# Kernel optimization log

Measured on AMD Instinct MI355X. Metric: run time of the kernel, lower is better.

The kernel has to match this reference:

```python
import jax, jax.numpy as jnp
import numpy as np
from jax import lax

SCORE_THRESHOLD = 0.5
IOU_THRESHOLD = 0.5
N_ANCHORS = 8400


def setup_inputs() -> dict:
    key = jax.random.key(0)
    yolo_raw_output = jax.random.uniform(key, (1, 5, N_ANCHORS), dtype=jnp.float32)
    return {"yolo_raw_output": yolo_raw_output}


def _pairwise_iou(boxes):
    # boxes: [N, 4] in xyxy
    x1, y1, x2, y2 = boxes[:, 0], boxes[:, 1], boxes[:, 2], boxes[:, 3]
    area = (x2 - x1) * (y2 - y1)                       # [N]
    lt_x = jnp.maximum(x1[:, None], x1[None, :])       # [N, N]
    lt_y = jnp.maximum(y1[:, None], y1[None, :])
    rb_x = jnp.minimum(x2[:, None], x2[None, :])
    rb_y = jnp.minimum(y2[:, None], y2[None, :])
    inter = jnp.clip(rb_x - lt_x, 0.0) * jnp.clip(rb_y - lt_y, 0.0)
    union = area[:, None] + area[None, :] - inter
    return inter / union


def reference(yolo_raw_output):
    # [1, 5, N] -> [N, 5]
    out = jnp.transpose(yolo_raw_output, (0, 2, 1))[0]
    scores = out[:, 4]
    valid = scores > SCORE_THRESHOLD            # score filter (mask, fixed shape)

    # cxcywh -> xyxy
    cx, cy, w, h = out[:, 0], out[:, 1], out[:, 2], out[:, 3]
    xyxy = jnp.stack([cx - w * 0.5, cy - h * 0.5, cx + w * 0.5, cy + h * 0.5], axis=1)

    # sort by score descending (invalid pushed to the end)
    masked_scores = jnp.where(valid, scores, -jnp.inf)
    order = jnp.argsort(-masked_scores)
    boxes_s = xyxy[order]                       # [N, 4]
    scores_s = jnp.where(valid, scores, 0.0)[order]
    valid_s = valid[order]

    # NMS: pairwise IoU + sequential suppression over sorted boxes
    iou = _pairwise_iou(lax.stop_gradient(boxes_s))
    suppress = iou > IOU_THRESHOLD              # [N, N] bool
    idx = jnp.arange(boxes_s.shape[0])

    def body(i, keep):
        # box i suppresses later boxes only if it itself is kept
        sup = suppress[i] & keep[i] & (idx > i)
        return keep & ~sup

    keep = lax.fori_loop(0, boxes_s.shape[0], body, valid_s)

    boxes_and_scores = jnp.concatenate([boxes_s, scores_s[:, None]], axis=1)  # [N, 5]
    # fixed-shape analogue of boxes_and_scores[selected_indices]:
    # suppressed / below-threshold rows are zeroed, kept rows are score-sorted.
    return jnp.where(keep[:, None], boxes_and_scores, 0.0)
```

## Files before the change

### kernel.cpp

```cpp
#include <hip/hip_runtime.h>
#include <cstdint>

#define N_ANCH 8400
#define WMAX   132
#define NB     (WMAX * 64)
#define NT     128

__device__ __forceinline__ uint64_t readlane64(uint64_t v, int lane) {
  unsigned lo = (unsigned)__builtin_amdgcn_readlane((int)(unsigned)(v & 0xffffffffull), lane);
  unsigned hi = (unsigned)__builtin_amdgcn_readlane((int)(unsigned)(v >> 32), lane);
  return ((uint64_t)hi << 32) | lo;
}

__global__ __launch_bounds__(256) void k_rank(const float* __restrict__ in,
                                              float* __restrict__ scores_s,
                                              float4* __restrict__ boxes_s,
                                              unsigned* __restrict__ nvp) {
  __shared__ alignas(16) float sc[N_ANCH];
  __shared__ int part[256];
  const int tid = threadIdx.x;
  const float* srow = in + 4 * N_ANCH;
  for (int j = tid; j < N_ANCH; j += 256) sc[j] = srow[j];
  __syncthreads();
  const int il = tid & 63, q = tid >> 6;
  const int i = blockIdx.x * 64 + il;
  const float si = (i < N_ANCH) ? sc[i] : 0.0f;
  const bool valid = si > 0.5f;
  const float key = valid ? si : -INFINITY;
  int cnt = 0;
  const float4* sc4 = (const float4*)sc;
  const int jb = q * (N_ANCH / 4);
  for (int jj = 0; jj < (N_ANCH / 16); ++jj) {
    float4 v = sc4[q * (N_ANCH / 16) + jj];
    int j0 = jb + jj * 4;
    float k0 = (v.x > 0.5f) ? v.x : -INFINITY;
    float k1 = (v.y > 0.5f) ? v.y : -INFINITY;
    float k2 = (v.z > 0.5f) ? v.z : -INFINITY;
    float k3 = (v.w > 0.5f) ? v.w : -INFINITY;
    cnt += (k0 > key) || (k0 == key && (j0 + 0) < i);
    cnt += (k1 > key) || (k1 == key && (j0 + 1) < i);
    cnt += (k2 > key) || (k2 == key && (j0 + 2) < i);
    cnt += (k3 > key) || (k3 == key && (j0 + 3) < i);
  }
  part[tid] = cnt;
  __syncthreads();
  if (q == 0 && i < N_ANCH) {
    int r = part[il] + part[64 + il] + part[128 + il] + part[192 + il];
    float cx = in[0 * N_ANCH + i], cy = in[1 * N_ANCH + i];
    float w  = in[2 * N_ANCH + i], h  = in[3 * N_ANCH + i];
    float x1 = cx - w * 0.5f, y1 = cy - h * 0.5f;
    float x2 = cx + w * 0.5f, y2 = cy + h * 0.5f;
    boxes_s[r] = make_float4(x1, y1, x2, y2);
    scores_s[r] = valid ? si : 0.0f;
    if (valid) atomicAdd(nvp, 1u);
  }
}

__global__ __launch_bounds__(256) void k_sup(const float4* __restrict__ boxes_s,
                                             const unsigned* __restrict__ nvp,
                                             unsigned long long* __restrict__ sup,
                                             unsigned long long* __restrict__ diag) {
  const int nv = (int)*nvp;
  const int W = (nv + 63) >> 6;
  const int w = blockIdx.x;
  if (w >= W) return;
  __shared__ float bx1[64], by1[64], bx2[64], by2[64], bar[64];
  const int tid = threadIdx.x;
  if (tid < 64) {
    int j = w * 64 + tid;
    float4 b = (j < N_ANCH) ? boxes_s[j] : make_float4(0.f, 0.f, 0.f, 0.f);
    bx1[tid] = b.x; by1[tid] = b.y; bx2[tid] = b.z; by2[tid] = b.w;
    bar[tid] = (b.z - b.x) * (b.w - b.y);
  }
  __syncthreads();
  const int i = blockIdx.y * 256 + tid;
  if (i >= nv) return;
  float4 bi = boxes_s[i];
  float ai = (bi.z - bi.x) * (bi.w - bi.y);
  const int jmax = nv - w * 64;
  uint64_t bits = 0;
  #pragma unroll 8
  for (int l = 0; l < 64; ++l) {
    float lx = fmaxf(bi.x, bx1[l]);
    float ly = fmaxf(bi.y, by1[l]);
    float rx = fminf(bi.z, bx2[l]);
    float ry = fminf(bi.w, by2[l]);
    float dx = fmaxf(rx - lx, 0.0f);
    float dy = fmaxf(ry - ly, 0.0f);
    float inter = dx * dy;
    asm volatile("" : "+v"(inter));
    float uni = (ai + bar[l]) - inter;
    float iou = inter / uni;
    bits |= ((uint64_t)((l < jmax) && (iou > 0.5f))) << l;
  }
  sup[(size_t)i * W + w] = bits;
  if (w == (i >> 6)) diag[i] = bits;
}

__global__ __launch_bounds__(NT) void k_scan(const float* __restrict__ scores_s,
                                             const float4* __restrict__ boxes_s,
                                             const unsigned long long* __restrict__ sup_,
                                             const unsigned long long* __restrict__ diag_g,
                                             const unsigned* __restrict__ nvp,
                                             float* __restrict__ out) {
  __shared__ uint64_t keep_s[WMAX];
  const uint64_t* sup = (const uint64_t*)sup_;
  const int tid = threadIdx.x;
  const int lane = tid & 63;
  const int q = tid >> 6;
  const int nv = (int)*nvp;
  const int W  = (nv + 63) >> 6;

  for (int idx = tid; idx < WMAX; idx += NT) {
    uint64_t v = 0; int base = idx * 64;
    if (base < nv) { int rem = nv - base; v = (rem >= 64) ? ~0ull : ((1ull << rem) - 1ull); }
    keep_s[idx] = v;
  }

  uint64_t dw = 0;
  if (q == 0 && W > 0) dw = (uint64_t)diag_g[lane];
  __syncthreads();

  for (int k = 0; k < W; ++k) {
    if (q == 0) {
      uint64_t cur = dw;
      if (k + 1 < W) dw = (uint64_t)diag_g[(size_t)(k + 1) * 64 + lane];
      uint64_t bk = keep_s[k];
      uint64_t cand = bk;
      while (cand) {
        int r = (int)__builtin_ctzll(cand);
        uint64_t sr = readlane64(cur, r);
        uint64_t m = sr & ~((2ull << r) - 1ull);
        cand &= ~(1ull << r);
        cand &= ~m;
        bk   &= ~m;
      }
      if (lane == 0) keep_s[k] = bk;
    }
    __syncthreads();

    const uint64_t bk2 = keep_s[k];
    if (bk2) {
      const int rowbase = k * 64;
      for (int wd = k + 1 + tid; wd < W; wd += NT) {
        uint64_t acc = 0;
        uint64_t rem = bk2;
        while (rem) {
          int r0, r1, r2, r3, r4, r5, r6, r7;
          uint64_t m0, m1, m2, m3, m4, m5, m6, m7;
          r0 = (int)__builtin_ctzll(rem); rem &= rem - 1;
          m1 = (uint64_t)0 - (uint64_t)(rem != 0);
          r1 = rem ? (int)__builtin_ctzll(rem) : r0; rem &= rem - 1;
          m2 = (uint64_t)0 - (uint64_t)(rem != 0);
          r2 = rem ? (int)__builtin_ctzll(rem) : r0; rem &= rem - 1;
          m3 = (uint64_t)0 - (uint64_t)(rem != 0);
          r3 = rem ? (int)__builtin_ctzll(rem) : r0; rem &= rem - 1;
          m4 = (uint64_t)0 - (uint64_t)(rem != 0);
          r4 = rem ? (int)__builtin_ctzll(rem) : r0; rem &= rem - 1;
          m5 = (uint64_t)0 - (uint64_t)(rem != 0);
          r5 = rem ? (int)__builtin_ctzll(rem) : r0; rem &= rem - 1;
          m6 = (uint64_t)0 - (uint64_t)(rem != 0);
          r6 = rem ? (int)__builtin_ctzll(rem) : r0; rem &= rem - 1;
          m7 = (uint64_t)0 - (uint64_t)(rem != 0);
          r7 = rem ? (int)__builtin_ctzll(rem) : r0; rem &= rem - 1;
          uint64_t v0 = sup[(size_t)(rowbase + r0) * W + wd];
          uint64_t v1 = sup[(size_t)(rowbase + r1) * W + wd];
          uint64_t v2 = sup[(size_t)(rowbase + r2) * W + wd];
          uint64_t v3 = sup[(size_t)(rowbase + r3) * W + wd];
          uint64_t v4 = sup[(size_t)(rowbase + r4) * W + wd];
          uint64_t v5 = sup[(size_t)(rowbase + r5) * W + wd];
          uint64_t v6 = sup[(size_t)(rowbase + r6) * W + wd];
          uint64_t v7 = sup[(size_t)(rowbase + r7) * W + wd];
          acc |= v0 | (v1 & m1) | (v2 & m2) | (v3 & m3)
                    | (v4 & m4) | (v5 & m5) | (v6 & m6) | (v7 & m7);
        }
        keep_s[wd] &= ~acc;
      }
    }
    __syncthreads();
  }

  for (int r = tid; r < N_ANCH; r += NT) {
    bool kept = (r < nv) && ((keep_s[r >> 6] >> (r & 63)) & 1ull);
    float4 b = kept ? boxes_s[r] : make_float4(0.f, 0.f, 0.f, 0.f);
    float s = kept ? scores_s[r] : 0.0f;
    out[r * 5 + 0] = b.x;
    out[r * 5 + 1] = b.y;
    out[r * 5 + 2] = b.z;
    out[r * 5 + 3] = b.w;
    out[r * 5 + 4] = s;
  }
}

extern "C" void kernel_launch(void* const* d_in, const int* in_sizes, int n_in,
                              void* d_out, int out_size, void* d_ws, size_t ws_size,
                              hipStream_t stream) {
  const float* in = (const float*)d_in[0];
  float* out = (float*)d_out;
  uint8_t* ws = (uint8_t*)d_ws;
  unsigned* nvp = (unsigned*)ws;
  float* scores_s = (float*)(ws + 64);
  float4* boxes_s = (float4*)(ws + 64 + 33600);
  unsigned long long* diag = (unsigned long long*)(ws + 64 + 33600 + (size_t)NB * 16);
  unsigned long long* sup  = (unsigned long long*)(ws + 64 + 33600 + (size_t)NB * 24);

  hipMemsetAsync(ws, 0, 64, stream);
  k_rank<<<dim3(WMAX), dim3(256), 0, stream>>>(in, scores_s, boxes_s, nvp);
  k_sup<<<dim3(WMAX, (N_ANCH + 255) / 256), dim3(256), 0, stream>>>(boxes_s, nvp, sup, diag);
  k_scan<<<dim3(1), dim3(NT), 0, stream>>>(scores_s, boxes_s, sup, diag, nvp, out);
}
```

Before: 258.0 us.

## Stage suppression-mask panels into LDS with async global_load_lds pipeline in NMS scan

The serial scan kernel now uses 512 threads and a three-stage software pipeline. For future word-blocks it copies the rows of still-kept candidates, plus the diagonal block, directly into LDS using global_load_lds. This removes the dependent global-memory latency that each serial step paid when OR-ing suppression rows. The suppression matrix row stride is padded to an even width so the 16-byte loads stay aligned. A fallback path keeps the old scheme when W exceeds 80 words, at the cost of roughly 128KB of LDS, hand-placed waitcnt and barrier synchronisation, and extra dummy loads.

Result: slower. 346.3 us (+34.2%).

```diff
diff --git a/kernel.cpp b/kernel.cpp
--- a/kernel.cpp
+++ b/kernel.cpp
@@ -4,12 +4,21 @@
 #define N_ANCH 8400
 #define WMAX   132
 #define NB     (WMAX * 64)
-#define NT     128
+#define NT     512
+#define NWAVE  8
+#define NI     9
+#define WLIM   80
+#define STRIDEW 82
 
 __device__ __forceinline__ uint64_t readlane64(uint64_t v, int lane) {
   unsigned lo = (unsigned)__builtin_amdgcn_readlane((int)(unsigned)(v & 0xffffffffull), lane);
   unsigned hi = (unsigned)__builtin_amdgcn_readlane((int)(unsigned)(v >> 32), lane);
   return ((uint64_t)hi << 32) | lo;
+}
+
+__device__ __forceinline__ void gl16(const void* g, void* l) {
+  __builtin_amdgcn_global_load_lds((const __attribute__((address_space(1))) uint32_t*)g,
+                                   (__attribute__((address_space(3))) uint32_t*)l, 16, 0, 0);
 }
 
 __global__ __launch_bounds__(256) void k_rank(const float* __restrict__ in,
@@ -62,6 +71,7 @@
                                              unsigned long long* __restrict__ diag) {
   const int nv = (int)*nvp;
   const int W = (nv + 63) >> 6;
+  const int Wp = (W + 1) & ~1;
   const int w = blockIdx.x;
   if (w >= W) return;
   __shared__ float bx1[64], by1[64], bx2[64], by2[64], bar[64];
@@ -93,7 +103,7 @@
     float iou = inter / uni;
     bits |= ((uint64_t)((l < jmax) && (iou > 0.5f))) << l;
   }
-  sup[(size_t)i * W + w] = bits;
+  sup[(size_t)i * Wp + w] = bits;
   if (w == (i >> 6)) diag[i] = bits;
 }
 
@@ -104,81 +114,163 @@
                                              const unsigned* __restrict__ nvp,
                                              float* __restrict__ out) {
   __shared__ uint64_t keep_s[WMAX];
+  __shared__ uint64_t pan[3][64 * STRIDEW];
+  __shared__ uint64_t diag_lds[3][64];
+  __shared__ uint64_t dump[128];
+  __shared__ unsigned rowbit[3][64];
+  __shared__ unsigned slotmap[3][64];
+  __shared__ unsigned ncand[3];
   const uint64_t* sup = (const uint64_t*)sup_;
+  const uint64_t* diag64 = (const uint64_t*)diag_g;
   const int tid = threadIdx.x;
   const int lane = tid & 63;
   const int q = tid >> 6;
   const int nv = (int)*nvp;
   const int W  = (nv + 63) >> 6;
+  const int Wp = (W + 1) & ~1;
 
   for (int idx = tid; idx < WMAX; idx += NT) {
     uint64_t v = 0; int base = idx * 64;
     if (base < nv) { int rem = nv - base; v = (rem >= 64) ? ~0ull : ((1ull << rem) - 1ull); }
     keep_s[idx] = v;
   }
-
-  uint64_t dw = 0;
-  if (q == 0 && W > 0) dw = (uint64_t)diag_g[lane];
-  __syncthreads();
-
-  for (int k = 0; k < W; ++k) {
-    if (q == 0) {
-      uint64_t cur = dw;
-      if (k + 1 < W) dw = (uint64_t)diag_g[(size_t)(k + 1) * 64 + lane];
-      uint64_t bk = keep_s[k];
-      uint64_t cand = bk;
-      while (cand) {
-        int r = (int)__builtin_ctzll(cand);
-        uint64_t sr = readlane64(cur, r);
-        uint64_t m = sr & ~((2ull << r) - 1ull);
-        cand &= ~(1ull << r);
-        cand &= ~m;
-        bk   &= ~m;
-      }
-      if (lane == 0) keep_s[k] = bk;
+  __syncthreads();
+
+  if (W > 0 && W <= WLIM) {
+    auto extract = [&](int K) {
+      const int stg = K % 3;
+      if (K >= W) { if (lane == 0) ncand[stg] = 0; return; }
+      uint64_t word = keep_s[K];
+      int set = (int)((word >> lane) & 1ull);
+      unsigned slot = (unsigned)__popcll(word & ((1ull << lane) - 1ull));
+      if (set) rowbit[stg][slot] = (unsigned)lane;
+      slotmap[stg][lane] = set ? slot : 0xFFFFFFFFu;
+      if (lane == 0) ncand[stg] = (unsigned)__popcll(word);
+    };
+    auto issue_batch = [&](int K) {
+      const int stg = K % 3;
+      const int se = (K + 1) & ~1;
+      const int nhalf = (W > se) ? ((W - se + 1) >> 1) : 0;
+      const int nc = (K < W) ? (int)ncand[stg] : 0;
+      #pragma unroll 1
+      for (int j = 0; j < NI; ++j) {
+        int s = q * NI + j;
+        const uint64_t* gp; uint64_t* lp; int lim;
+        if (s == 0 && K < W) {
+          gp = diag64 + (size_t)K * 64 + 2 * lane;
+          lp = &diag_lds[stg][0];
+          lim = 32;
+        } else if (s >= 1 && s <= 64 && (s - 1) < nc && nhalf > 0) {
+          int rb = (int)rowbit[stg][s - 1];
+          size_t row = (size_t)K * 64 + rb;
+          gp = sup + row * Wp + se + 2 * lane;
+          lp = &pan[stg][(size_t)(s - 1) * STRIDEW];
+          lim = nhalf;
+        } else {
+          gp = sup + 2 * lane;
+          lp = &dump[0];
+          lim = 64;
+        }
+        if (lane < lim) gl16(gp, lp);
+      }
+    };
+
+    if (q == 0) extract(0);
+    else if (q == 1) extract(1);
+    asm volatile("s_waitcnt lgkmcnt(0)" ::: "memory");
+    __builtin_amdgcn_sched_barrier(0);
+    __builtin_amdgcn_s_barrier();
+    __builtin_amdgcn_sched_barrier(0);
+    issue_batch(0);
+    issue_batch(1);
+
+    for (int k = 0; k < W; ++k) {
+      asm volatile("s_waitcnt vmcnt(9) lgkmcnt(0)" ::: "memory");
+      __builtin_amdgcn_sched_barrier(0);
+      __builtin_amdgcn_s_barrier();
+      __builtin_amdgcn_sched_barrier(0);
+
+      if (q == 0) {
+        uint64_t cur = diag_lds[k % 3][lane];
+        uint64_t bk = keep_s[k];
+        uint64_t cand = bk;
+        while (cand) {
+          int r = (int)__builtin_ctzll(cand);
+          uint64_t sr = readlane64(cur, r);
+          uint64_t m = sr & ~((2ull << r) - 1ull);
+          cand &= ~(1ull << r);
+          cand &= ~m;
+          bk   &= ~m;
+        }
+        if (lane == 0) keep_s[k] = bk;
+      } else if (q == 1) {
+        extract(k + 2);
+      }
+      asm volatile("s_waitcnt lgkmcnt(0)" ::: "memory");
+      __builtin_amdgcn_sched_barrier(0);
+      __builtin_amdgcn_s_barrier();
+      __builtin_amdgcn_sched_barrier(0);
+
+      issue_batch(k + 2);
+
+      {
+        uint64_t bk2 = keep_s[k];
+        int wd = k + 1 + tid;
+        if (bk2 && wd < W) {
+          const int stg = k % 3;
+          const int se = (k + 1) & ~1;
+          uint64_t acc = 0;
+          uint64_t rem = bk2;
+          while (rem) {
+            int r = (int)__builtin_ctzll(rem);
+            rem &= rem - 1;
+            unsigned slot = slotmap[stg][r];
+            acc |= pan[stg][(size_t)slot * STRIDEW + (wd - se)];
+          }
+          keep_s[wd] &= ~acc;
+        }
+      }
+      asm volatile("s_waitcnt lgkmcnt(0)" ::: "memory");
+      __builtin_amdgcn_sched_barrier(0);
+      __builtin_amdgcn_s_barrier();
+      __builtin_amdgcn_sched_barrier(0);
     }
+    asm volatile("s_waitcnt vmcnt(0)" ::: "memory");
+  } else if (W > 0) {
+    uint64_t dw = 0;
+    if (q == 0) dw = (uint64_t)diag_g[lane];
     __syncthreads();
-
-    const uint64_t bk2 = keep_s[k];
-    if (bk2) {
-      const int rowbase = k * 64;
-      for (int wd = k + 1 + tid; wd < W; wd += NT) {
-        uint64_t acc = 0;
-        uint64_t rem = bk2;
-        while (rem) {
-          int r0, r1, r2, r3, r4, r5, r6, r7;
-          uint64_t m0, m1, m2, m3, m4, m5, m6, m7;
-          r0 = (int)__builtin_ctzll(rem); rem &= rem - 1;
-          m1 = (uint64_t)0 - (uint64_t)(rem != 0);
-          r1 = rem ? (int)__builtin_ctzll(rem) : r0; rem &= rem - 1;
-          m2 = (uint64_t)0 - (uint64_t)(rem != 0);
-          r2 = rem ? (int)__builtin_ctzll(rem) : r0; rem &= rem - 1;
-          m3 = (uint64_t)0 - (uint64_t)(rem != 0);
-          r3 = rem ? (int)__builtin_ctzll(rem) : r0; rem &= rem - 1;
-          m4 = (uint64_t)0 - (uint64_t)(rem != 0);
-          r4 = rem ? (int)__builtin_ctzll(rem) : r0; rem &= rem - 1;
-          m5 = (uint64_t)0 - (uint64_t)(rem != 0);
-          r5 = rem ? (int)__builtin_ctzll(rem) : r0; rem &= rem - 1;
-          m6 = (uint64_t)0 - (uint64_t)(rem != 0);
-          r6 = rem ? (int)__builtin_ctzll(rem) : r0; rem &= rem - 1;
-          m7 = (uint64_t)0 - (uint64_t)(rem != 0);
-          r7 = rem ? (int)__builtin_ctzll(rem) : r0; rem &= rem - 1;
-          uint64_t v0 = sup[(size_t)(rowbase + r0) * W + wd];
-          uint64_t v1 = sup[(size_t)(rowbase + r1) * W + wd];
-          uint64_t v2 = sup[(size_t)(rowbase + r2) * W + wd];
-          uint64_t v3 = sup[(size_t)(rowbase + r3) * W + wd];
-          uint64_t v4 = sup[(size_t)(rowbase + r4) * W + wd];
-          uint64_t v5 = sup[(size_t)(rowbase + r5) * W + wd];
-          uint64_t v6 = sup[(size_t)(rowbase + r6) * W + wd];
-          uint64_t v7 = sup[(size_t)(rowbase + r7) * W + wd];
-          acc |= v0 | (v1 & m1) | (v2 & m2) | (v3 & m3)
-                    | (v4 & m4) | (v5 & m5) | (v6 & m6) | (v7 & m7);
-        }
-        keep_s[wd] &= ~acc;
-      }
+    for (int k = 0; k < W; ++k) {
+      if (q == 0) {
+        uint64_t cur = dw;
+        if (k + 1 < W) dw = (uint64_t)diag_g[(size_t)(k + 1) * 64 + lane];
+        uint64_t bk = keep_s[k];
+        uint64_t cand = bk;
+        while (cand) {
+          int r = (int)__builtin_ctzll(cand);
+          uint64_t sr = readlane64(cur, r);
+          uint64_t m = sr & ~((2ull << r) - 1ull);
+          cand &= ~(1ull << r); cand &= ~m; bk &= ~m;
+        }
+        if (lane == 0) keep_s[k] = bk;
+      }
+      __syncthreads();
+      const uint64_t bk2 = keep_s[k];
+      if (bk2) {
+        const int rowbase = k * 64;
+        for (int wd = k + 1 + tid; wd < W; wd += NT) {
+          uint64_t acc = 0, rem = bk2;
+          while (rem) {
+            int r = (int)__builtin_ctzll(rem); rem &= rem - 1;
+            acc |= sup[(size_t)(rowbase + r) * Wp + wd];
+          }
+          keep_s[wd] &= ~acc;
+        }
+      }
+      __syncthreads();
     }
-    __syncthreads();
-  }
+  }
+  __syncthreads();
 
   for (int r = tid; r < N_ANCH; r += NT) {
     bool kept = (r < nv) && ((keep_s[r >> 6] >> (r & 63)) & 1ull);
@@ -204,7 +296,7 @@
   unsigned long long* diag = (unsigned long long*)(ws + 64 + 33600 + (size_t)NB * 16);
   unsigned long long* sup  = (unsigned long long*)(ws + 64 + 33600 + (size_t)NB * 24);
 
-  hipMemsetAsync(ws, 0, 64, stream);
+  (void)hipMemsetAsync(ws, 0, 64, stream);
   k_rank<<<dim3(WMAX), dim3(256), 0, stream>>>(in, scores_s, boxes_s, nvp);
   k_sup<<<dim3(WMAX, (N_ANCH + 255) / 256), dim3(256), 0, stream>>>(boxes_s, nvp, sup, diag);
   k_scan<<<dim3(1), dim3(NT), 0, stream>>>(scores_s, boxes_s, sup, diag, nvp, out);
```

## Run NMS scan in a single wave with prefetched suppression rows

Applied to the files above, without the earlier changes.

The sequential NMS scan now runs entirely in one wavefront, dropping the two block barriers per 64-box word. It prefetches up to 32 suppression words per lane for the next word before they are needed, and handles far columns with a wave-wide OR reduction. The suppression-mask kernel also skips blocks and threads below the diagonal, which the scan never reads, and pads the row stride to an even count. The cost is higher register pressure from the prefetch array and serial per-column loops when there are many words. The other waves sit idle until the final output write.

Result: slower. 284.9 us (+10.4%).

```diff
diff --git a/kernel.cpp b/kernel.cpp
--- a/kernel.cpp
+++ b/kernel.cpp
@@ -4,12 +4,23 @@
 #define N_ANCH 8400
 #define WMAX   132
 #define NB     (WMAX * 64)
-#define NT     128
+#define NT     512
+#define CSLOT  32
 
 __device__ __forceinline__ uint64_t readlane64(uint64_t v, int lane) {
   unsigned lo = (unsigned)__builtin_amdgcn_readlane((int)(unsigned)(v & 0xffffffffull), lane);
   unsigned hi = (unsigned)__builtin_amdgcn_readlane((int)(unsigned)(v >> 32), lane);
   return ((uint64_t)hi << 32) | lo;
+}
+__device__ __forceinline__ uint64_t firstlane64(uint64_t v) {
+  unsigned lo = (unsigned)__builtin_amdgcn_readfirstlane((int)(unsigned)(v & 0xffffffffull));
+  unsigned hi = (unsigned)__builtin_amdgcn_readfirstlane((int)(unsigned)(v >> 32));
+  return ((uint64_t)hi << 32) | lo;
+}
+__device__ __forceinline__ uint64_t shflxor64(uint64_t v, int m) {
+  int lo = __shfl_xor((int)(unsigned)(v & 0xffffffffull), m, 64);
+  int hi = __shfl_xor((int)(unsigned)(v >> 32), m, 64);
+  return ((uint64_t)(unsigned)hi << 32) | (unsigned)lo;
 }
 
 __global__ __launch_bounds__(256) void k_rank(const float* __restrict__ in,
@@ -62,8 +73,10 @@
                                              unsigned long long* __restrict__ diag) {
   const int nv = (int)*nvp;
   const int W = (nv + 63) >> 6;
+  const int Wp = (W + 1) & ~1;
   const int w = blockIdx.x;
   if (w >= W) return;
+  if (w + 1 < (int)(blockIdx.y * 256) >> 6) return;
   __shared__ float bx1[64], by1[64], bx2[64], by2[64], bar[64];
   const int tid = threadIdx.x;
   if (tid < 64) {
@@ -75,6 +88,7 @@
   __syncthreads();
   const int i = blockIdx.y * 256 + tid;
   if (i >= nv) return;
+  if (w < (i >> 6)) return;
   float4 bi = boxes_s[i];
   float ai = (bi.z - bi.x) * (bi.w - bi.y);
   const int jmax = nv - w * 64;
@@ -93,7 +107,7 @@
     float iou = inter / uni;
     bits |= ((uint64_t)((l < jmax) && (iou > 0.5f))) << l;
   }
-  sup[(size_t)i * W + w] = bits;
+  sup[(size_t)i * Wp + w] = bits;
   if (w == (i >> 6)) diag[i] = bits;
 }
 
@@ -105,80 +119,128 @@
                                              float* __restrict__ out) {
   __shared__ uint64_t keep_s[WMAX];
   const uint64_t* sup = (const uint64_t*)sup_;
+  const uint64_t* diag64 = (const uint64_t*)diag_g;
   const int tid = threadIdx.x;
   const int lane = tid & 63;
-  const int q = tid >> 6;
+  const int wave = tid >> 6;
   const int nv = (int)*nvp;
   const int W  = (nv + 63) >> 6;
+  const int Wp = (W + 1) & ~1;
 
   for (int idx = tid; idx < WMAX; idx += NT) {
     uint64_t v = 0; int base = idx * 64;
     if (base < nv) { int rem = nv - base; v = (rem >= 64) ? ~0ull : ((1ull << rem) - 1ull); }
     keep_s[idx] = v;
   }
-
-  uint64_t dw = 0;
-  if (q == 0 && W > 0) dw = (uint64_t)diag_g[lane];
-  __syncthreads();
-
-  for (int k = 0; k < W; ++k) {
-    if (q == 0) {
-      uint64_t cur = dw;
-      if (k + 1 < W) dw = (uint64_t)diag_g[(size_t)(k + 1) * 64 + lane];
-      uint64_t bk = keep_s[k];
-      uint64_t cand = bk;
-      while (cand) {
-        int r = (int)__builtin_ctzll(cand);
-        uint64_t sr = readlane64(cur, r);
-        uint64_t m = sr & ~((2ull << r) - 1ull);
-        cand &= ~(1ull << r);
-        cand &= ~m;
-        bk   &= ~m;
+  __syncthreads();
+
+  if (wave == 0 && W > 0) {
+    uint64_t pre[CSLOT];
+    uint64_t bkw = firstlane64(keep_s[0]);
+    uint64_t ovw = 0;
+    uint64_t dw  = diag64[lane];
+
+    {
+      uint64_t remc = bkw;
+      const int wd = 1 + lane;
+      #pragma unroll
+      for (int s = 0; s < CSLOT; ++s) {
+        int r = remc ? (int)__builtin_ctzll(remc) : 0;
+        bool valid = (remc != 0);
+        remc &= remc - 1;
+        pre[s] = (valid && wd < W) ? sup[(size_t)r * Wp + wd] : 0ull;
+      }
+      ovw = remc;
+    }
+
+    for (int k = 0; k < W; ++k) {
+      uint64_t bk = bkw;
+      {
+        uint64_t cand = bk;
+        while (cand) {
+          int r = (int)__builtin_ctzll(cand);
+          uint64_t sr = readlane64(dw, r);
+          uint64_t m = sr & ~((2ull << r) - 1ull);
+          cand &= ~(1ull << r);
+          cand &= ~m;
+          bk   &= ~m;
+        }
       }
       if (lane == 0) keep_s[k] = bk;
+      if (k + 1 < W) dw = diag64[(size_t)(k + 1) * 64 + lane];
+
+      const int wd = k + 1 + lane;
+      uint64_t acc = 0;
+      {
+        uint64_t remc = bkw;
+        #pragma unroll
+        for (int s = 0; s < CSLOT; ++s) {
+          int r = remc ? (int)__builtin_ctzll(remc) : 0;
+          uint64_t mk = (uint64_t)0 - (uint64_t)((remc != 0) && ((bk >> r) & 1ull));
+          remc &= remc - 1;
+          acc |= pre[s] & mk;
+        }
+      }
+      {
+        uint64_t remo = ovw & bk;
+        const size_t rowbase = (size_t)k * 64;
+        while (remo) {
+          int r0 = (int)__builtin_ctzll(remo); remo &= remo - 1;
+          uint64_t m1 = (uint64_t)0 - (uint64_t)(remo != 0);
+          int r1 = remo ? (int)__builtin_ctzll(remo) : r0; remo &= remo - 1;
+          uint64_t m2 = (uint64_t)0 - (uint64_t)(remo != 0);
+          int r2 = remo ? (int)__builtin_ctzll(remo) : r0; remo &= remo - 1;
+          uint64_t m3 = (uint64_t)0 - (uint64_t)(remo != 0);
+          int r3 = remo ? (int)__builtin_ctzll(remo) : r0; remo &= remo - 1;
+          uint64_t m4 = (uint64_t)0 - (uint64_t)(remo != 0);
+          int r4 = remo ? (int)__builtin_ctzll(remo) : r0; remo &= remo - 1;
+          uint64_t m5 = (uint64_t)0 - (uint64_t)(remo != 0);
+          int r5 = remo ? (int)__builtin_ctzll(remo) : r0; remo &= remo - 1;
+          uint64_t m6 = (uint64_t)0 - (uint64_t)(remo != 0);
+          int r6 = remo ? (int)__builtin_ctzll(remo) : r0; remo &= remo - 1;
+          uint64_t m7 = (uint64_t)0 - (uint64_t)(remo != 0);
+          int r7 = remo ? (int)__builtin_ctzll(remo) : r0; remo &= remo - 1;
+          if (wd < W) {
+            uint64_t v0 = sup[(rowbase + r0) * Wp + wd];
+            uint64_t v1 = sup[(rowbase + r1) * Wp + wd];
+            uint64_t v2 = sup[(rowbase + r2) * Wp + wd];
+            uint64_t v3 = sup[(rowbase + r3) * Wp + wd];
+            uint64_t v4 = sup[(rowbase + r4) * Wp + wd];
+            uint64_t v5 = sup[(rowbase + r5) * Wp + wd];
+            uint64_t v6 = sup[(rowbase + r6) * Wp + wd];
+            uint64_t v7 = sup[(rowbase + r7) * Wp + wd];
+            acc |= v0 | (v1 & m1) | (v2 & m2) | (v3 & m3)
+                      | (v4 & m4) | (v5 & m5) | (v6 & m6) | (v7 & m7);
+          }
+        }
+      }
+      if (wd < W) keep_s[wd] &= ~acc;
+
+      for (int wd2 = k + 65; wd2 < W; ++wd2) {
+        uint64_t v = 0;
+        if ((bk >> lane) & 1ull) v = sup[((size_t)k * 64 + lane) * Wp + wd2];
+        v |= shflxor64(v, 1);  v |= shflxor64(v, 2);  v |= shflxor64(v, 4);
+        v |= shflxor64(v, 8);  v |= shflxor64(v, 16); v |= shflxor64(v, 32);
+        if (lane == 0) keep_s[wd2] &= ~v;
+      }
+
+      if (k + 1 < W) {
+        bkw = firstlane64(keep_s[k + 1]);
+        uint64_t remc = bkw;
+        const int wdn = k + 2 + lane;
+        const size_t rb = (size_t)(k + 1) * 64;
+        #pragma unroll
+        for (int s = 0; s < CSLOT; ++s) {
+          int r = remc ? (int)__builtin_ctzll(remc) : 0;
+          bool valid = (remc != 0);
+          remc &= remc - 1;
+          pre[s] = (valid && wdn < W) ? sup[(rb + r) * Wp + wdn] : 0ull;
+        }
+        ovw = remc;
+      }
     }
-    __syncthreads();
-
-    const uint64_t bk2 = keep_s[k];
-    if (bk2) {
-      const int rowbase = k * 64;
-      for (int wd = k + 1 + tid; wd < W; wd += NT) {
-        uint64_t acc = 0;
-        uint64_t rem = bk2;
-        while (rem) {
-          int r0, r1, r2, r3, r4, r5, r6, r7;
-          uint64_t m0, m1, m2, m3, m4, m5, m6, m7;
-          r0 = (int)__builtin_ctzll(rem); rem &= rem - 1;
-          m1 = (uint64_t)0 - (uint64_t)(rem != 0);
-          r1 = rem ? (int)__builtin_ctzll(rem) : r0; rem &= rem - 1;
-          m2 = (uint64_t)0 - (uint64_t)(rem != 0);
-          r2 = rem ? (int)__builtin_ctzll(rem) : r0; rem &= rem - 1;
-          m3 = (uint64_t)0 - (uint64_t)(rem != 0);
-          r3 = rem ? (int)__builtin_ctzll(rem) : r0; rem &= rem - 1;
-          m4 = (uint64_t)0 - (uint64_t)(rem != 0);
-          r4 = rem ? (int)__builtin_ctzll(rem) : r0; rem &= rem - 1;
-          m5 = (uint64_t)0 - (uint64_t)(rem != 0);
-          r5 = rem ? (int)__builtin_ctzll(rem) : r0; rem &= rem - 1;
-          m6 = (uint64_t)0 - (uint64_t)(rem != 0);
-          r6 = rem ? (int)__builtin_ctzll(rem) : r0; rem &= rem - 1;
-          m7 = (uint64_t)0 - (uint64_t)(rem != 0);
-          r7 = rem ? (int)__builtin_ctzll(rem) : r0; rem &= rem - 1;
-          uint64_t v0 = sup[(size_t)(rowbase + r0) * W + wd];
-          uint64_t v1 = sup[(size_t)(rowbase + r1) * W + wd];
-          uint64_t v2 = sup[(size_t)(rowbase + r2) * W + wd];
-          uint64_t v3 = sup[(size_t)(rowbase + r3) * W + wd];
-          uint64_t v4 = sup[(size_t)(rowbase + r4) * W + wd];
-          uint64_t v5 = sup[(size_t)(rowbase + r5) * W + wd];
-          uint64_t v6 = sup[(size_t)(rowbase + r6) * W + wd];
-          uint64_t v7 = sup[(size_t)(rowbase + r7) * W + wd];
-          acc |= v0 | (v1 & m1) | (v2 & m2) | (v3 & m3)
-                    | (v4 & m4) | (v5 & m5) | (v6 & m6) | (v7 & m7);
-        }
-        keep_s[wd] &= ~acc;
-      }
-    }
-    __syncthreads();
-  }
+  }
+  __syncthreads();
 
   for (int r = tid; r < N_ANCH; r += NT) {
     bool kept = (r < nv) && ((keep_s[r >> 6] >> (r & 63)) & 1ull);
@@ -204,7 +266,7 @@
   unsigned long long* diag = (unsigned long long*)(ws + 64 + 33600 + (size_t)NB * 16);
   unsigned long long* sup  = (unsigned long long*)(ws + 64 + 33600 + (size_t)NB * 24);
 
-  hipMemsetAsync(ws, 0, 64, stream);
+  (void)hipMemsetAsync(ws, 0, 64, stream);
   k_rank<<<dim3(WMAX), dim3(256), 0, stream>>>(in, scores_s, boxes_s, nvp);
   k_sup<<<dim3(WMAX, (N_ANCH + 255) / 256), dim3(256), 0, stream>>>(boxes_s, nvp, sup, diag);
   k_scan<<<dim3(1), dim3(NT), 0, stream>>>(scores_s, boxes_s, sup, diag, nvp, out);
```
